# Kernel tuning notes

Hardware: AMD Instinct MI355X
Metric: run time of the kernel (lower is better)

The kernel has to match this reference:

```python
import jax, jax.numpy as jnp
import numpy as np

EMBED_DIM = 10
CHEB_K = 2
DIM_IN = 64
DIM_OUT = 64
BATCH = 64
NUM_NODES = 4096


def setup_inputs() -> dict:
    key = jax.random.key(0)
    k1, k2, k3 = jax.random.split(key, 3)
    x = jax.random.normal(k1, (BATCH, NUM_NODES, DIM_IN), dtype=jnp.float32)
    node_embeddings = jax.random.normal(k2, (NUM_NODES, EMBED_DIM), dtype=jnp.float32)
    # xavier-uniform-like init for weights_pool, zeros for bias_pool
    fan_in = EMBED_DIM * CHEB_K * DIM_IN
    fan_out = DIM_OUT
    limit = float(np.sqrt(6.0 / (fan_in + fan_out)))
    weights_pool = jax.random.uniform(k3, (EMBED_DIM, CHEB_K, DIM_IN, DIM_OUT), dtype=jnp.float32, minval=-limit, maxval=limit)
    bias_pool = jnp.zeros((EMBED_DIM, DIM_OUT), dtype=jnp.float32)
    return {"x": x, "node_embeddings": node_embeddings, "weights_pool": weights_pool, "bias_pool": bias_pool}


def reference(x, node_embeddings, weights_pool, bias_pool):
    num_nodes = x.shape[1]
    # adaptive support: softmax(relu(E E^T)) over last dim  [N, N]
    sim = jax.nn.relu(node_embeddings @ node_embeddings.T)
    supports1 = jax.nn.softmax(sim, axis=-1)
    eye = jnp.eye(num_nodes, dtype=x.dtype)
    supports = jnp.stack([eye, supports1], axis=0)  # [k, N, N]
    # per-node weights and bias from node embeddings
    weights = jnp.einsum('nd,dkio->nkio', node_embeddings, weights_pool)  # [N, k, Ci, Co]
    bias = node_embeddings @ bias_pool  # [N, Co]
    # graph diffusion: [k, N, M] x [B, M, Ci] -> [B, N, k, Ci]
    x_g = jnp.einsum('knm,bmc->bnkc', supports, x)
    # per-node GEMM: [B, N, k, Ci] x [N, k, Ci, Co] -> [B, N, Co]
    x_gconv = jnp.einsum('bnki,nkio->bno', x_g, weights) + bias
    return x_gconv
```

## Files before the change

### kernel.cpp

```cpp
#include <hip/hip_runtime.h>
#include <cstdint>
#include <cstddef>

#define N_NODES 4096
#define EMB 10
#define BATCH_SZ 64
#define CI 64
#define CO 64
#define LKP 136

typedef unsigned short u16;
typedef __bf16 bf16x8 __attribute__((ext_vector_type(8)));
typedef float f32x4 __attribute__((ext_vector_type(4)));

__device__ __forceinline__ u16 f2bf(float f) {
  union { float f; uint32_t u; } v; v.f = f;
  const uint32_t r = v.u + 0x7fffu + ((v.u >> 16) & 1u);
  return (u16)(r >> 16);
}

__device__ __forceinline__ void gload16(const void* g, void* l) {
  __builtin_amdgcn_global_load_lds(
      (__attribute__((address_space(1))) void*)(g),
      (__attribute__((address_space(3))) void*)(l), 16, 0, 0);
}

__global__ __launch_bounds__(256) void support_softmax(
    const float* __restrict__ E, u16* __restrict__ Sb) {
  __shared__ float sim[4][N_NODES];
  __shared__ float EnS[4][EMB];
  __shared__ float red[4][4];
  const int n0 = blockIdx.x * 4;
  const int t = threadIdx.x;
  const int wid = t >> 6;
  if (t < 4 * EMB) EnS[t / EMB][t % EMB] = E[n0 * EMB + t];
  __syncthreads();
  float en[4][EMB];
#pragma unroll
  for (int r = 0; r < 4; ++r)
#pragma unroll
    for (int d = 0; d < EMB; ++d) en[r][d] = EnS[r][d];

  float rmax[4] = {-1e30f, -1e30f, -1e30f, -1e30f};
  for (int p = 0; p < 16; ++p) {
    const int m = p * 256 + t;
    const float2* e2 = reinterpret_cast<const float2*>(E + m * EMB);
    float em[EMB];
    const float2 v0 = e2[0], v1 = e2[1], v2 = e2[2], v3 = e2[3], v4 = e2[4];
    em[0] = v0.x; em[1] = v0.y; em[2] = v1.x; em[3] = v1.y; em[4] = v2.x;
    em[5] = v2.y; em[6] = v3.x; em[7] = v3.y; em[8] = v4.x; em[9] = v4.y;
#pragma unroll
    for (int r = 0; r < 4; ++r) {
      float acc = 0.f;
#pragma unroll
      for (int d = 0; d < EMB; ++d) acc += en[r][d] * em[d];
      acc = fmaxf(acc, 0.f);
      sim[r][m] = acc;
      rmax[r] = fmaxf(rmax[r], acc);
    }
  }
#pragma unroll
  for (int r = 0; r < 4; ++r) {
#pragma unroll
    for (int s = 32; s; s >>= 1) rmax[r] = fmaxf(rmax[r], __shfl_xor(rmax[r], s));
  }
  if ((t & 63) == 0) {
#pragma unroll
    for (int r = 0; r < 4; ++r) red[r][wid] = rmax[r];
  }
  __syncthreads();
  float gmax[4];
#pragma unroll
  for (int r = 0; r < 4; ++r)
    gmax[r] = fmaxf(fmaxf(red[r][0], red[r][1]), fmaxf(red[r][2], red[r][3]));
  __syncthreads();

  float rsum[4] = {0.f, 0.f, 0.f, 0.f};
  for (int p = 0; p < 16; ++p) {
    const int m = p * 256 + t;
#pragma unroll
    for (int r = 0; r < 4; ++r) {
      const float e = __expf(sim[r][m] - gmax[r]);
      sim[r][m] = e;
      rsum[r] += e;
    }
  }
#pragma unroll
  for (int r = 0; r < 4; ++r) {
#pragma unroll
    for (int s = 32; s; s >>= 1) rsum[r] += __shfl_xor(rsum[r], s);
  }
  if ((t & 63) == 0) {
#pragma unroll
    for (int r = 0; r < 4; ++r) red[r][wid] = rsum[r];
  }
  __syncthreads();
  float inv[4];
#pragma unroll
  for (int r = 0; r < 4; ++r)
    inv[r] = 1.0f / (red[r][0] + red[r][1] + red[r][2] + red[r][3]);

  for (int p = 0; p < 16; ++p) {
    const int m = p * 256 + t;
#pragma unroll
    for (int r = 0; r < 4; ++r)
      Sb[(size_t)(n0 + r) * N_NODES + m] = f2bf(sim[r][m] * inv[r]);
  }
}

__global__ __launch_bounds__(256) void convert_x(
    const float* __restrict__ x, u16* __restrict__ Xt) {
  __shared__ float sm[64][65];
  const int b = blockIdx.x, mt = blockIdx.y;
  const int t = threadIdx.x;
  const int c = t & 63, q = t >> 6;
  const float* xp = x + ((size_t)b * N_NODES + mt * 64) * CI;
#pragma unroll
  for (int p = 0; p < 16; ++p) {
    const int r = q + p * 4;
    sm[r][c] = xp[(size_t)r * CI + c];
  }
  __syncthreads();
  u16* op = Xt + (size_t)(b * 64) * N_NODES + mt * 64;
#pragma unroll
  for (int p = 0; p < 16; ++p) {
    const int cc = q + p * 4;
    op[(size_t)cc * N_NODES + c] = f2bf(sm[c][cc]);
  }
}

__global__ __launch_bounds__(256) void diffuse_gemm_mfma(
    const u16* __restrict__ S, const u16* __restrict__ Xt,
    u16* __restrict__ Zb) {
  __shared__ __align__(16) u16 As[128 * 64];
  __shared__ __align__(16) u16 Bs[128 * 64];
  const int t = threadIdx.x;
  const int lane = t & 63;
  const int w = t >> 6;
  const int wm = w >> 1, wn = w & 1;
  const int n0 = blockIdx.y * 128;
  const int j0 = blockIdx.x * 128;

  const int srow = w * 32 + (lane >> 3);
  const int scol = (lane & 7) * 8;
  const u16* gA = S  + (size_t)(n0 + srow) * N_NODES + scol;
  const u16* gB = Xt + (size_t)(j0 + srow) * N_NODES + scol;
  u16* lA = &As[(w * 32) * 64];
  u16* lB = &Bs[(w * 32) * 64];

  f32x4 acc[4][4];
#pragma unroll
  for (int i = 0; i < 4; ++i)
#pragma unroll
    for (int j = 0; j < 4; ++j) acc[i][j] = (f32x4)0.f;

  const int fr = lane & 15;
  const int fk = (lane >> 4) * 8;

  for (int kt = 0; kt < N_NODES / 64; ++kt) {
    const size_t ko = (size_t)kt * 64;
#pragma unroll
    for (int q = 0; q < 4; ++q) {
      gload16(gA + ko + (size_t)(q * 8) * N_NODES, lA + q * 512);
      gload16(gB + ko + (size_t)(q * 8) * N_NODES, lB + q * 512);
    }
    __syncthreads();
#pragma unroll
    for (int ks = 0; ks < 2; ++ks) {
      bf16x8 a[4], b[4];
#pragma unroll
      for (int fm = 0; fm < 4; ++fm)
        a[fm] = *reinterpret_cast<const bf16x8*>(
            &As[(wm * 64 + fm * 16 + fr) * 64 + ks * 32 + fk]);
#pragma unroll
      for (int fn = 0; fn < 4; ++fn)
        b[fn] = *reinterpret_cast<const bf16x8*>(
            &Bs[(wn * 64 + fn * 16 + fr) * 64 + ks * 32 + fk]);
#pragma unroll
      for (int fm = 0; fm < 4; ++fm)
#pragma unroll
        for (int fn = 0; fn < 4; ++fn)
          acc[fm][fn] = __builtin_amdgcn_mfma_f32_16x16x32_bf16(
              a[fm], b[fn], acc[fm][fn], 0, 0, 0);
    }
    __syncthreads();
  }

  const int crow = (lane >> 4) * 4;
  const int ccol = lane & 15;
#pragma unroll
  for (int fm = 0; fm < 4; ++fm) {
    const int nrow = n0 + wm * 64 + fm * 16 + crow;
#pragma unroll
    for (int fn = 0; fn < 4; ++fn) {
      const int jcol = j0 + wn * 64 + fn * 16 + ccol;
#pragma unroll
      for (int r = 0; r < 4; ++r)
        Zb[(size_t)(nrow + r) * N_NODES + jcol] = f2bf(acc[fm][fn][r]);
    }
  }
}

__global__ __launch_bounds__(256) void node_gemm_mfma(
    const float* __restrict__ x, const u16* __restrict__ Zb,
    const float* __restrict__ E, const float* __restrict__ wp,
    const float* __restrict__ bp, float* __restrict__ out) {
  __shared__ __align__(16) u16 Wt[2][64][LKP];
  __shared__ __align__(16) u16 Axz[2][64][LKP];
  __shared__ float biasS[2][64];
  __shared__ float EnS[2][EMB];
  const int n0 = blockIdx.x * 2;
  const int t = threadIdx.x;
  const int lane = t & 63;
  const int w = t >> 6;
  if (t < 2 * EMB) EnS[t / EMB][t % EMB] = E[n0 * EMB + t];
  __syncthreads();
  float en0[EMB], en1[EMB];
#pragma unroll
  for (int d = 0; d < EMB; ++d) { en0[d] = EnS[0][d]; en1[d] = EnS[1][d]; }

  if (t < 128) {
    const int nn = t >> 6, o = t & 63;
    float b = 0.f;
#pragma unroll
    for (int d = 0; d < EMB; ++d) b += EnS[nn][d] * bp[d * CO + o];
    biasS[nn][o] = b;
  }

  const float4* wp4 = reinterpret_cast<const float4*>(wp);
#pragma unroll
  for (int p = 0; p < 8; ++p) {
    const int e4 = p * 256 + t;
    const int ki = e4 >> 4, o4 = e4 & 15;
    float a0x = 0.f, a0y = 0.f, a0z = 0.f, a0w = 0.f;
    float a1x = 0.f, a1y = 0.f, a1z = 0.f, a1w = 0.f;
#pragma unroll
    for (int d = 0; d < EMB; ++d) {
      const float4 wv = wp4[d * 2048 + e4];
      a0x += en0[d] * wv.x; a0y += en0[d] * wv.y;
      a0z += en0[d] * wv.z; a0w += en0[d] * wv.w;
      a1x += en1[d] * wv.x; a1y += en1[d] * wv.y;
      a1z += en1[d] * wv.z; a1w += en1[d] * wv.w;
    }
    Wt[0][o4 * 4 + 0][ki] = f2bf(a0x); Wt[0][o4 * 4 + 1][ki] = f2bf(a0y);
    Wt[0][o4 * 4 + 2][ki] = f2bf(a0z); Wt[0][o4 * 4 + 3][ki] = f2bf(a0w);
    Wt[1][o4 * 4 + 0][ki] = f2bf(a1x); Wt[1][o4 * 4 + 1][ki] = f2bf(a1y);
    Wt[1][o4 * 4 + 2][ki] = f2bf(a1z); Wt[1][o4 * 4 + 3][ki] = f2bf(a1w);
  }

#pragma unroll
  for (int nn = 0; nn < 2; ++nn) {
    const int ng = n0 + nn;
#pragma unroll
    for (int pb = 0; pb < 4; ++pb) {
      const int b = pb * 16 + (t >> 4);
      const int i0 = (t & 15) * 4;
      const float4 xv = *reinterpret_cast<const float4*>(
          &x[(size_t)b * (N_NODES * CI) + (size_t)ng * CI + i0]);
      ushort4 uv;
      uv.x = f2bf(xv.x); uv.y = f2bf(xv.y); uv.z = f2bf(xv.z); uv.w = f2bf(xv.w);
      *reinterpret_cast<ushort4*>(&Axz[nn][b][i0]) = uv;
    }
#pragma unroll
    for (int pz = 0; pz < 4; ++pz) {
      const int t4 = pz * 256 + t;
      const int b = t4 >> 4, c0 = (t4 & 15) * 4;
      const ushort4 zv = *reinterpret_cast<const ushort4*>(
          &Zb[(size_t)ng * N_NODES + t4 * 4]);
      *reinterpret_cast<ushort4*>(&Axz[nn][b][64 + c0]) = zv;
    }
  }
  __syncthreads();

  const int nn = w >> 1, bh = w & 1;
  const int fr = lane & 15, fk = (lane >> 4) * 8;
  f32x4 acc[2][4];
#pragma unroll
  for (int m = 0; m < 2; ++m)
#pragma unroll
    for (int n = 0; n < 4; ++n) acc[m][n] = (f32x4)0.f;

#pragma unroll
  for (int kk = 0; kk < 4; ++kk) {
    bf16x8 a[2], b[4];
#pragma unroll
    for (int m = 0; m < 2; ++m)
      a[m] = *reinterpret_cast<const bf16x8*>(
          &Axz[nn][bh * 32 + m * 16 + fr][kk * 32 + fk]);
#pragma unroll
    for (int n = 0; n < 4; ++n)
      b[n] = *reinterpret_cast<const bf16x8*>(
          &Wt[nn][n * 16 + fr][kk * 32 + fk]);
#pragma unroll
    for (int m = 0; m < 2; ++m)
#pragma unroll
      for (int n = 0; n < 4; ++n)
        acc[m][n] = __builtin_amdgcn_mfma_f32_16x16x32_bf16(
            a[m], b[n], acc[m][n], 0, 0, 0);
  }

  const int crow = (lane >> 4) * 4;
  const int ccol = lane & 15;
  const int ng = n0 + nn;
#pragma unroll
  for (int m = 0; m < 2; ++m) {
#pragma unroll
    for (int n = 0; n < 4; ++n) {
      const int o = n * 16 + ccol;
      const float bv = biasS[nn][o];
#pragma unroll
      for (int r = 0; r < 4; ++r) {
        const int b = bh * 32 + m * 16 + crow + r;
        out[(size_t)b * (N_NODES * CI) + (size_t)ng * CI + o] =
            acc[m][n][r] + bv;
      }
    }
  }
}

extern "C" void kernel_launch(void* const* d_in, const int* in_sizes, int n_in,
                              void* d_out, int out_size, void* d_ws, size_t ws_size,
                              hipStream_t stream) {
  const float* x  = (const float*)d_in[0];
  const float* E  = (const float*)d_in[1];
  const float* wp = (const float*)d_in[2];
  const float* bp = (const float*)d_in[3];
  float* out = (float*)d_out;
  const size_t MAT = (size_t)N_NODES * N_NODES;
  u16* Sb = (u16*)d_ws;
  u16* Xt = Sb + MAT;
  u16* Zb = Xt + MAT;

  support_softmax<<<N_NODES / 4, 256, 0, stream>>>(E, Sb);
  convert_x<<<dim3(BATCH_SZ, N_NODES / 64), 256, 0, stream>>>(x, Xt);
  diffuse_gemm_mfma<<<dim3(32, 32), 256, 0, stream>>>(Sb, Xt, Zb);
  node_gemm_mfma<<<N_NODES / 2, 256, 0, stream>>>(x, Zb, E, wp, bp, out);
}
```

Baseline: 360.5 us.

## Pipeline diffusion GEMM with triple-buffered LDS, larger tiles, and swizzled layout

```diff
diff --git a/kernel.cpp b/kernel.cpp
--- a/kernel.cpp
+++ b/kernel.cpp
@@ -8,6 +8,11 @@
 #define CI 64
 #define CO 64
 #define LKP 136
+
+#define BM 256
+#define BN 128
+#define SLOT_U16 24576
+#define BOFF_U16 16384
 
 typedef unsigned short u16;
 typedef __bf16 bf16x8 __attribute__((ext_vector_type(8)));
@@ -129,24 +134,42 @@
   }
 }
 
-__global__ __launch_bounds__(256) void diffuse_gemm_mfma(
+__global__ __launch_bounds__(512) void diffuse_gemm_pipe(
     const u16* __restrict__ S, const u16* __restrict__ Xt,
     u16* __restrict__ Zb) {
-  __shared__ __align__(16) u16 As[128 * 64];
-  __shared__ __align__(16) u16 Bs[128 * 64];
-  const int t = threadIdx.x;
-  const int lane = t & 63;
-  const int w = t >> 6;
+  __shared__ __align__(16) u16 lds[3 * SLOT_U16];
+  const int tid = threadIdx.x;
+  const int lane = tid & 63;
+  const int w = tid >> 6;
+  const int bid = blockIdx.x;
+  const int sw = (bid & 7) * 64 + (bid >> 3);
+  const int by = sw >> 5;
+  const int bx = sw & 31;
+  const int n0 = by * BM;
+  const int j0 = bx * BN;
+
+  const int lrow8 = lane >> 3;
+  const int scol = 8 * ((lane & 7) ^ lrow8);
+  const u16* gsrc[6];
+  const u16* lbase[6];
+#pragma unroll
+  for (int i = 0; i < 6; ++i) {
+    const int chunk = w * 6 + i;
+    if (chunk < 32) {
+      const int row = chunk * 8 + lrow8;
+      gsrc[i] = S + (size_t)(n0 + row) * N_NODES + scol;
+      lbase[i] = &lds[chunk * 512];
+    } else {
+      const int row = (chunk - 32) * 8 + lrow8;
+      gsrc[i] = Xt + (size_t)(j0 + row) * N_NODES + scol;
+      lbase[i] = &lds[BOFF_U16 + (chunk - 32) * 512];
+    }
+  }
+
   const int wm = w >> 1, wn = w & 1;
-  const int n0 = blockIdx.y * 128;
-  const int j0 = blockIdx.x * 128;
-
-  const int srow = w * 32 + (lane >> 3);
-  const int scol = (lane & 7) * 8;
-  const u16* gA = S  + (size_t)(n0 + srow) * N_NODES + scol;
-  const u16* gB = Xt + (size_t)(j0 + srow) * N_NODES + scol;
-  u16* lA = &As[(w * 32) * 64];
-  u16* lB = &Bs[(w * 32) * 64];
+  const int fr = lane & 15;
+  const int khalf = lane >> 4;
+  const int swz16 = (fr & 7) << 3;
 
   f32x4 acc[4][4];
 #pragma unroll
@@ -154,37 +177,63 @@
 #pragma unroll
     for (int j = 0; j < 4; ++j) acc[i][j] = (f32x4)0.f;
 
-  const int fr = lane & 15;
-  const int fk = (lane >> 4) * 8;
-
-  for (int kt = 0; kt < N_NODES / 64; ++kt) {
-    const size_t ko = (size_t)kt * 64;
-#pragma unroll
-    for (int q = 0; q < 4; ++q) {
-      gload16(gA + ko + (size_t)(q * 8) * N_NODES, lA + q * 512);
-      gload16(gB + ko + (size_t)(q * 8) * N_NODES, lB + q * 512);
-    }
-    __syncthreads();
-#pragma unroll
-    for (int ks = 0; ks < 2; ++ks) {
-      bf16x8 a[4], b[4];
-#pragma unroll
-      for (int fm = 0; fm < 4; ++fm)
-        a[fm] = *reinterpret_cast<const bf16x8*>(
-            &As[(wm * 64 + fm * 16 + fr) * 64 + ks * 32 + fk]);
-#pragma unroll
-      for (int fn = 0; fn < 4; ++fn)
-        b[fn] = *reinterpret_cast<const bf16x8*>(
-            &Bs[(wn * 64 + fn * 16 + fr) * 64 + ks * 32 + fk]);
-#pragma unroll
-      for (int fm = 0; fm < 4; ++fm)
-#pragma unroll
-        for (int fn = 0; fn < 4; ++fn)
-          acc[fm][fn] = __builtin_amdgcn_mfma_f32_16x16x32_bf16(
-              a[fm], b[fn], acc[fm][fn], 0, 0, 0);
-    }
-    __syncthreads();
-  }
+#define STAGE(tt)                                                         \
+  {                                                                       \
+    const int _s = (tt) % 3;                                              \
+    _Pragma("unroll")                                                     \
+    for (int i = 0; i < 6; ++i)                                           \
+      gload16(gsrc[i] + (size_t)(tt) * 64,                                \
+              (void*)(lbase[i] + _s * SLOT_U16));                         \
+  }
+
+#define COMPUTE(ss)                                                       \
+  {                                                                       \
+    const u16* sa = &lds[(ss) * SLOT_U16];                                \
+    const u16* sb = sa + BOFF_U16;                                        \
+    _Pragma("unroll")                                                     \
+    for (int ks = 0; ks < 2; ++ks) {                                      \
+      const int c16 = (ks * 32 + khalf * 8) ^ swz16;                      \
+      bf16x8 a[4], b[4];                                                  \
+      _Pragma("unroll")                                                   \
+      for (int fm = 0; fm < 4; ++fm)                                      \
+        a[fm] = *reinterpret_cast<const bf16x8*>(                         \
+            &sa[(wm * 64 + fm * 16 + fr) * 64 + c16]);                    \
+      _Pragma("unroll")                                                   \
+      for (int fn = 0; fn < 4; ++fn)                                      \
+        b[fn] = *reinterpret_cast<const bf16x8*>(                         \
+            &sb[(wn * 64 + fn * 16 + fr) * 64 + c16]);                    \
+      __builtin_amdgcn_s_setprio(1);                                      \
+      _Pragma("unroll")                                                   \
+      for (int fm = 0; fm < 4; ++fm)                                      \
+        _Pragma("unroll")                                                 \
+        for (int fn = 0; fn < 4; ++fn)                                    \
+          acc[fm][fn] = __builtin_amdgcn_mfma_f32_16x16x32_bf16(          \
+              a[fm], b[fn], acc[fm][fn], 0, 0, 0);                        \
+      __builtin_amdgcn_s_setprio(0);                                      \
+    }                                                                     \
+  }
+
+  STAGE(0);
+  STAGE(1);
+
+  int s = 0;
+  for (int t = 0; t < 62; ++t) {
+    asm volatile("s_waitcnt vmcnt(6)" ::: "memory");
+    __builtin_amdgcn_s_barrier();
+    __builtin_amdgcn_sched_barrier(0);
+    STAGE(t + 2);
+    COMPUTE(s);
+    s = (s == 2) ? 0 : s + 1;
+  }
+  asm volatile("s_waitcnt vmcnt(6)" ::: "memory");
+  __builtin_amdgcn_s_barrier();
+  __builtin_amdgcn_sched_barrier(0);
+  COMPUTE(s);
+  s = (s == 2) ? 0 : s + 1;
+  asm volatile("s_waitcnt vmcnt(0)" ::: "memory");
+  __builtin_amdgcn_s_barrier();
+  __builtin_amdgcn_sched_barrier(0);
+  COMPUTE(s);
 
   const int crow = (lane >> 4) * 4;
   const int ccol = lane & 15;
@@ -199,6 +248,8 @@
         Zb[(size_t)(nrow + r) * N_NODES + jcol] = f2bf(acc[fm][fn][r]);
     }
   }
+#undef STAGE
+#undef COMPUTE
 }
 
 __global__ __launch_bounds__(256) void node_gemm_mfma(
@@ -333,6 +384,6 @@
 
   support_softmax<<<N_NODES / 4, 256, 0, stream>>>(E, Sb);
   convert_x<<<dim3(BATCH_SZ, N_NODES / 64), 256, 0, stream>>>(x, Xt);
-  diffuse_gemm_mfma<<<dim3(32, 32), 256, 0, stream>>>(Sb, Xt, Zb);
+  diffuse_gemm_pipe<<<512, 512, 0, stream>>>(Sb, Xt, Zb);
   node_gemm_mfma<<<N_NODES / 2, 256, 0, stream>>>(x, Zb, E, wp, bp, out);
 }
```

Result: faster. 322.8 us (-10.4%).
